# Optimization experiments

Hardware: AMD Instinct MI355X
Metric: run time of the kernel (lower is better)

Reference implementation:

```python
import jax, jax.numpy as jnp
import numpy as np
import math

HEADS = 16
D_MODEL = 1024
EPS = 1e-5  # nn.LayerNorm default


def setup_inputs() -> dict:
    key = jax.random.key(0)
    ks = jax.random.split(key, 12)
    bs, s, d = 4, 2048, D_MODEL
    scale = 1.0 / math.sqrt(d)
    inp = {
        "q": jax.random.normal(ks[0], (bs, s, d), jnp.float32),
        "k": jax.random.normal(ks[1], (bs, s, d), jnp.float32),
        "v": jax.random.normal(ks[2], (bs, s, d), jnp.float32),
        # causal target mask, broadcast over batch; 0 => masked
        "trg_mask": jnp.broadcast_to(jnp.tril(jnp.ones((s, s), jnp.int32)), (bs, s, s)),
        "Wq": jax.random.normal(ks[3], (d, d), jnp.float32) * scale,
        "bq": jax.random.normal(ks[4], (d,), jnp.float32) * 0.01,
        "Wk": jax.random.normal(ks[5], (d, d), jnp.float32) * scale,
        "bk": jax.random.normal(ks[6], (d,), jnp.float32) * 0.01,
        "Wv": jax.random.normal(ks[7], (d, d), jnp.float32) * scale,
        "bv": jax.random.normal(ks[8], (d,), jnp.float32) * 0.01,
        "gamma": jnp.ones((d,), jnp.float32),
        "beta": jnp.zeros((d,), jnp.float32),
    }
    return inp


def _layer_norm(x, gamma, beta):
    mu = jnp.mean(x, axis=-1, keepdims=True)
    var = jnp.mean(jnp.square(x - mu), axis=-1, keepdims=True)
    return (x - mu) * jax.lax.rsqrt(var + EPS) * gamma + beta


def reference(q, k, v, trg_mask, Wq, bq, Wk, bk, Wv, bv, gamma, beta):
    bs, s, d = q.shape
    h, dk = HEADS, d // HEADS
    temp = q
    # nn.Linear: x @ W.T + b
    qp = (q @ Wq.T + bq).reshape(bs, s, h, dk)
    kp = (k @ Wk.T + bk).reshape(bs, s, h, dk)
    vp = (v @ Wv.T + bv).reshape(bs, s, h, dk)
    # scores [bs, h, s, s]
    scores = jnp.einsum('bqhd,bkhd->bhqk', qp, kp)
    # NOTE: original masks BEFORE dividing by sqrt(dk)
    scores = jnp.where(trg_mask[:, None, :, :] == 0, jnp.float32(-1e9), scores)
    attn = jax.nn.softmax(scores / math.sqrt(dk), axis=-1)
    ctx = jnp.einsum('bhqk,bkhd->bqhd', attn, vp).reshape(bs, s, d)
    # (cat over heads == transpose-back merge, identical math)
    return _layer_norm(ctx + temp, gamma, beta)
```

## Files before the change

### kernel.cpp

```cpp
#include <hip/hip_runtime.h>
#include <hip/hip_bf16.h>
#include <stdint.h>

#define BATCH 4
#define SEQ 2048
#define DMODEL 1024
#define HEADS 16
#define DKH 64
#define MTOT (BATCH * SEQ)

typedef float  fx4  __attribute__((ext_vector_type(4)));
typedef short  sx8  __attribute__((ext_vector_type(8)));
typedef __bf16 bx8  __attribute__((ext_vector_type(8)));
typedef unsigned short ux4 __attribute__((ext_vector_type(4)));
typedef unsigned int   ux2i __attribute__((ext_vector_type(2)));
typedef unsigned int   ux4i __attribute__((ext_vector_type(4)));

__device__ __forceinline__ fx4 mfma16(sx8 a, sx8 b, fx4 c) {
  return __builtin_amdgcn_mfma_f32_16x16x32_bf16(
      __builtin_bit_cast(bx8, a), __builtin_bit_cast(bx8, b), c, 0, 0, 0);
}

__device__ __forceinline__ unsigned short f2bf(float x) {
  return __builtin_bit_cast(unsigned short, __float2bfloat16(x));
}

__device__ __forceinline__ float bf2f(unsigned short u) {
  return __builtin_bit_cast(float, (uint32_t)u << 16);
}

__device__ __forceinline__ void gll16(const void* g, void* l) {
  __builtin_amdgcn_global_load_lds(
      (const __attribute__((address_space(1))) void*)g,
      (__attribute__((address_space(3))) void*)l, 16, 0, 0);
}

__global__ __launch_bounds__(256) void convert_w(
    const float* __restrict__ s0, const float* __restrict__ s1, const float* __restrict__ s2,
    unsigned short* __restrict__ d0, unsigned short* __restrict__ d1, unsigned short* __restrict__ d2) {
  const float* s = (blockIdx.y == 0) ? s0 : (blockIdx.y == 1) ? s1 : s2;
  unsigned short* d = (blockIdx.y == 0) ? d0 : (blockIdx.y == 1) ? d1 : d2;
  const int n4 = DMODEL * DMODEL / 4;
  for (int i = blockIdx.x * 256 + threadIdx.x; i < n4; i += gridDim.x * 256) {
    fx4 v = ((const fx4*)s)[i];
    ux4 o;
    o.x = f2bf(v.x); o.y = f2bf(v.y); o.z = f2bf(v.z); o.w = f2bf(v.w);
    ((ux4*)d)[i] = o;
  }
}

#define GBM 128
#define GBN 128
#define GBK 64
#define NBLK ((MTOT / GBM) * (DMODEL / GBN))

struct QkvArgs {
  const float* A[3];
  const unsigned short* B[3];
  const float* bias[3];
  unsigned short* C[3];
  float cscale[3];
};

__global__ __launch_bounds__(256) void gemm_qkv(QkvArgs args) {
  const int e = blockIdx.z;
  const float* __restrict__ A = args.A[e];
  const unsigned short* __restrict__ B = args.B[e];
  const float* __restrict__ bias = args.bias[e];
  unsigned short* __restrict__ C = args.C[e];
  const float cscale = args.cscale[e];

  const int lin = blockIdx.x;
  const int swz = (lin & 7) * (NBLK / 8) + (lin >> 3);
  const int m0 = (swz >> 3) * GBM;
  const int n0 = (swz & 7) * GBN;

  __shared__ unsigned short As[GBM][GBK];
  __shared__ unsigned short Bs[GBN][GBK];

  const int tid  = threadIdx.x;
  const int lane = tid & 63;
  const int wv   = tid >> 6;
  const int wm   = wv >> 1;
  const int wn   = wv & 1;
  const int g    = lane >> 4;
  const int l16  = lane & 15;

  fx4 acc[4][4];
#pragma unroll
  for (int m = 0; m < 4; ++m)
#pragma unroll
    for (int n = 0; n < 4; ++n) acc[m][n] = (fx4){0.f, 0.f, 0.f, 0.f};

  for (int kt = 0; kt < DMODEL / GBK; ++kt) {
    const int k0 = kt * GBK;
#pragma unroll
    for (int i = 0; i < 4; ++i) {
      const int c = i * 256 + tid;
      const int row = c >> 3, col8 = c & 7;
      gll16(B + (size_t)(n0 + row) * DMODEL + k0 + col8 * 8, &Bs[0][0] + c * 8);
    }
#pragma unroll
    for (int i = 0; i < 4; ++i) {
      const int c = i * 256 + tid;
      const int row = c >> 3, col8 = c & 7;
      const float* src = A + (size_t)(m0 + row) * DMODEL + k0 + col8 * 8;
      fx4 a0 = *(const fx4*)src;
      fx4 a1 = *(const fx4*)(src + 4);
      sx8 pk;
      pk[0] = (short)f2bf(a0.x); pk[1] = (short)f2bf(a0.y);
      pk[2] = (short)f2bf(a0.z); pk[3] = (short)f2bf(a0.w);
      pk[4] = (short)f2bf(a1.x); pk[5] = (short)f2bf(a1.y);
      pk[6] = (short)f2bf(a1.z); pk[7] = (short)f2bf(a1.w);
      *(sx8*)(&As[0][0] + c * 8) = pk;
    }
    __syncthreads();

    sx8 af[4][2], bfr[4][2];
#pragma unroll
    for (int m = 0; m < 4; ++m)
#pragma unroll
      for (int kc = 0; kc < 2; ++kc)
        af[m][kc] = *(const sx8*)(&As[wm * 64 + m * 16 + l16][kc * 32 + g * 8]);
#pragma unroll
    for (int n = 0; n < 4; ++n)
#pragma unroll
      for (int kc = 0; kc < 2; ++kc)
        bfr[n][kc] = *(const sx8*)(&Bs[wn * 64 + n * 16 + l16][kc * 32 + g * 8]);
#pragma unroll
    for (int kc = 0; kc < 2; ++kc)
#pragma unroll
      for (int m = 0; m < 4; ++m)
#pragma unroll
        for (int n = 0; n < 4; ++n)
          acc[m][n] = mfma16(af[m][kc], bfr[n][kc], acc[m][n]);
    __syncthreads();
  }

#pragma unroll
  for (int n = 0; n < 4; ++n) {
    const int gcol = n0 + wn * 64 + n * 16 + l16;
    const float bv = bias[gcol];
#pragma unroll
    for (int m = 0; m < 4; ++m) {
      const int grow = m0 + wm * 64 + m * 16 + g * 4;
#pragma unroll
      for (int r = 0; r < 4; ++r)
        C[(size_t)(grow + r) * DMODEL + gcol] = f2bf((acc[m][n][r] + bv) * cscale);
    }
  }
}

#define QBLK 128
#define KVB 64
#define NQT (SEQ / QBLK)
#define DEFER_THR 8.0f

__global__ __launch_bounds__(256) void attn(const unsigned short* __restrict__ qp,
                                            const unsigned short* __restrict__ kp,
                                            const unsigned short* __restrict__ vp,
                                            unsigned short* __restrict__ ctx) {
  const int gid = blockIdx.x;
  const int hb  = gid & 63;
  const int h   = hb >> 2;
  const int b   = hb & 3;
  const int qt  = (NQT - 1) - (gid >> 6);

  __shared__ unsigned short Ks[2][KVB][DKH];
  __shared__ unsigned short Vs[2][KVB * DKH];
  __shared__ unsigned short Ps[4][32][KVB + 2];

  const int tid  = threadIdx.x;
  const int lane = tid & 63;
  const int wv   = tid >> 6;
  const int g    = lane >> 4;
  const int l16  = lane & 15;

  const size_t bh = ((size_t)b * SEQ) * DMODEL + (size_t)h * DKH;
  const int sbase = (lane & 48) + ((lane & 48) >> 2);

  const int q0  = qt * QBLK;
  const int ntl = 2 * (qt + 1);
  const int wq0 = q0 + wv * 32;

  sx8 qf[2][2];
#pragma unroll
  for (int m = 0; m < 2; ++m)
#pragma unroll
    for (int kc = 0; kc < 2; ++kc)
      qf[m][kc] = *(const sx8*)(qp + bh + (size_t)(wq0 + m * 16 + l16) * DMODEL + kc * 32 + g * 8);

  fx4 oacc[2][4];
  float mrow[2], lrow[2];
#pragma unroll
  for (int m = 0; m < 2; ++m) {
#pragma unroll
    for (int nt = 0; nt < 4; ++nt) oacc[m][nt] = (fx4){0.f, 0.f, 0.f, 0.f};
    mrow[m] = -1e30f; lrow[m] = 0.f;
  }

#pragma unroll
  for (int i = 0; i < 2; ++i) {
    const int c = i * 256 + tid;
    {
      const int row = c >> 3, col8 = c & 7;
      gll16(kp + bh + (size_t)row * DMODEL + (col8 ^ (row & 7)) * 8, &Ks[0][0][0] + c * 8);
    }
    {
      const int kv = ((c >> 5) << 2) | ((c >> 1) & 3);
      const int d0 = (((c >> 3) & 3) << 4) | ((c & 1) << 3);
      gll16(vp + bh + (size_t)kv * DMODEL + d0, &Vs[0][0] + c * 8);
    }
  }
  __syncthreads();

  int cur = 0;
  for (int t = 0; t < ntl; ++t) {
    const int kv0 = t * KVB;

    if (t + 1 < ntl) {
#pragma unroll
      for (int i = 0; i < 2; ++i) {
        const int c = i * 256 + tid;
        {
          const int row = c >> 3, col8 = c & 7;
          gll16(kp + bh + (size_t)(kv0 + KVB + row) * DMODEL + (col8 ^ (row & 7)) * 8,
                &Ks[cur ^ 1][0][0] + c * 8);
        }
        {
          const int kv = ((c >> 5) << 2) | ((c >> 1) & 3);
          const int d0 = (((c >> 3) & 3) << 4) | ((c & 1) << 3);
          gll16(vp + bh + (size_t)(kv0 + KVB + kv) * DMODEL + d0, &Vs[cur ^ 1][0] + c * 8);
        }
      }
    }

    sx8 kf[4][2];
#pragma unroll
    for (int nt = 0; nt < 4; ++nt) {
      const int row = l16 + 16 * nt;
#pragma unroll
      for (int kc = 0; kc < 2; ++kc)
        kf[nt][kc] = *(const sx8*)(&Ks[cur][row][((kc * 4 + g) ^ (row & 7)) * 8]);
    }
    fx4 st[2][4];
#pragma unroll
    for (int m = 0; m < 2; ++m)
#pragma unroll
      for (int nt = 0; nt < 4; ++nt) st[m][nt] = (fx4){0.f, 0.f, 0.f, 0.f};
    __builtin_amdgcn_s_setprio(1);
#pragma unroll
    for (int kc = 0; kc < 2; ++kc)
#pragma unroll
      for (int m = 0; m < 2; ++m)
#pragma unroll
        for (int nt = 0; nt < 4; ++nt)
          st[m][nt] = mfma16(kf[nt][kc], qf[m][kc], st[m][nt]);
    __builtin_amdgcn_s_setprio(0);

    bool mlive[2];
#pragma unroll
    for (int m = 0; m < 2; ++m) {
      mlive[m] = (kv0 <= wq0 + m * 16 + 15);
      if (!mlive[m]) continue;
      const int qrow = wq0 + m * 16 + l16;
      if (kv0 + KVB - 1 > wq0 + m * 16) {
#pragma unroll
        for (int nt = 0; nt < 4; ++nt)
#pragma unroll
          for (int r = 0; r < 4; ++r) {
            const int kvc = kv0 + nt * 16 + g * 4 + r;
            st[m][nt][r] = (kvc <= qrow) ? st[m][nt][r] : -1e30f;
          }
      }
      float mx = -1e30f;
#pragma unroll
      for (int nt = 0; nt < 4; ++nt)
#pragma unroll
        for (int r = 0; r < 4; ++r) mx = fmaxf(mx, st[m][nt][r]);
      mx = fmaxf(mx, __shfl_xor(mx, 16));
      mx = fmaxf(mx, __shfl_xor(mx, 32));

      if (!__all(mx <= mrow[m] + DEFER_THR)) {
        const float mnew = fmaxf(mrow[m], mx);
        const float corr = exp2f(mrow[m] - mnew);
        mrow[m] = mnew;
        lrow[m] *= corr;
        float c4[4];
#pragma unroll
        for (int r = 0; r < 4; ++r) c4[r] = __shfl(corr, sbase + r, 64);
#pragma unroll
        for (int nt = 0; nt < 4; ++nt)
#pragma unroll
          for (int r = 0; r < 4; ++r) oacc[m][nt][r] *= c4[r];
      }

      float rsum = 0.f;
#pragma unroll
      for (int nt = 0; nt < 4; ++nt)
#pragma unroll
        for (int r = 0; r < 4; ++r) {
          const float p = exp2f(st[m][nt][r] - mrow[m]);
          st[m][nt][r] = p;
          rsum += p;
        }
      rsum += __shfl_xor(rsum, 16);
      rsum += __shfl_xor(rsum, 32);
      lrow[m] += rsum;

      const int prow = m * 16 + l16;
      char* psrow = (char*)&Ps[wv][prow][0];
#pragma unroll
      for (int nt = 0; nt < 4; ++nt)
#pragma unroll
        for (int rr = 0; rr < 2; ++rr) {
          const uint32_t pk = (uint32_t)f2bf(st[m][nt][2 * rr]) |
                              ((uint32_t)f2bf(st[m][nt][2 * rr + 1]) << 16);
          *(uint32_t*)(psrow + ((nt * 2 + (g >> 1)) ^ (prow & 7)) * 16 + (g & 1) * 8 + rr * 4) = pk;
        }
    }

    const uint32_t vsb = (uint32_t)(uintptr_t)&Vs[cur][0];
#pragma unroll
    for (int kc = 0; kc < 2; ++kc) {
      sx8 vf[4];
#pragma unroll
      for (int nt = 0; nt < 4; ++nt) {
        const uint32_t a = vsb + (uint32_t)((kc * 8 + g * 2) * 512 + nt * 128 + l16 * 8);
        ux2i r0, r1;
        asm volatile("ds_read_b64_tr_b16 %0, %2\n\t"
                     "ds_read_b64_tr_b16 %1, %2 offset:512"
                     : "=&v"(r0), "=&v"(r1) : "v"(a));
        ux4i tmp;
        tmp[0] = r0[0]; tmp[1] = r0[1]; tmp[2] = r1[0]; tmp[3] = r1[1];
        vf[nt] = __builtin_bit_cast(sx8, tmp);
      }
      asm volatile("s_waitcnt lgkmcnt(0)" ::: "memory");
      __builtin_amdgcn_sched_barrier(0);
      __builtin_amdgcn_s_setprio(1);
#pragma unroll
      for (int m = 0; m < 2; ++m) {
        if (!mlive[m]) continue;
        const int prow = m * 16 + l16;
        sx8 pf = *(const sx8*)(&Ps[wv][prow][((kc * 4 + g) ^ (prow & 7)) * 8]);
#pragma unroll
        for (int nt = 0; nt < 4; ++nt)
          oacc[m][nt] = mfma16(pf, vf[nt], oacc[m][nt]);
      }
      __builtin_amdgcn_s_setprio(0);
    }

    __syncthreads();
    cur ^= 1;
  }

#pragma unroll
  for (int m = 0; m < 2; ++m) {
    const float inv = 1.0f / lrow[m];
    float i4[4];
#pragma unroll
    for (int r = 0; r < 4; ++r) i4[r] = __shfl(inv, sbase + r, 64);
#pragma unroll
    for (int nt = 0; nt < 4; ++nt)
#pragma unroll
      for (int r = 0; r < 4; ++r)
        ctx[bh + (size_t)(wq0 + m * 16 + g * 4 + r) * DMODEL + nt * 16 + l16] =
            f2bf(oacc[m][nt][r] * i4[r]);
  }
}

__global__ __launch_bounds__(256) void ln_kernel(const unsigned short* __restrict__ ctxb,
                                                 const float* __restrict__ qin,
                                                 float* __restrict__ out,
                                                 const float* __restrict__ gamma,
                                                 const float* __restrict__ beta) {
  const int row = blockIdx.x;
  const int tid = threadIdx.x;
  const unsigned short* crow = ctxb + (size_t)row * DMODEL;
  const float* qr = qin + (size_t)row * DMODEL;
  float* orow = out + (size_t)row * DMODEL;

  ux4 cv = ((const ux4*)crow)[tid];
  fx4 qv = ((const fx4*)qr)[tid];
  fx4 x;
  x.x = bf2f(cv.x) + qv.x;
  x.y = bf2f(cv.y) + qv.y;
  x.z = bf2f(cv.z) + qv.z;
  x.w = bf2f(cv.w) + qv.w;

  float s  = x.x + x.y + x.z + x.w;
  float ss = x.x * x.x + x.y * x.y + x.z * x.z + x.w * x.w;
#pragma unroll
  for (int off = 1; off < 64; off <<= 1) {
    s  += __shfl_xor(s, off);
    ss += __shfl_xor(ss, off);
  }
  __shared__ float rs[4], rss[4];
  if ((tid & 63) == 0) { rs[tid >> 6] = s; rss[tid >> 6] = ss; }
  __syncthreads();
  s  = rs[0] + rs[1] + rs[2] + rs[3];
  ss = rss[0] + rss[1] + rss[2] + rss[3];

  const float mu   = s * (1.0f / DMODEL);
  const float var  = ss * (1.0f / DMODEL) - mu * mu;
  const float rstd = rsqrtf(var + 1e-5f);

  fx4 gv = ((const fx4*)gamma)[tid];
  fx4 bv = ((const fx4*)beta)[tid];
  fx4 o;
  o.x = (x.x - mu) * rstd * gv.x + bv.x;
  o.y = (x.y - mu) * rstd * gv.y + bv.y;
  o.z = (x.z - mu) * rstd * gv.z + bv.z;
  o.w = (x.w - mu) * rstd * gv.w + bv.w;
  ((fx4*)orow)[tid] = o;
}

extern "C" void kernel_launch(void* const* d_in, const int* in_sizes, int n_in,
                              void* d_out, int out_size, void* d_ws, size_t ws_size,
                              hipStream_t stream) {
  const float* q     = (const float*)d_in[0];
  const float* k     = (const float*)d_in[1];
  const float* v     = (const float*)d_in[2];
  const float* Wq    = (const float*)d_in[4];
  const float* bq    = (const float*)d_in[5];
  const float* Wk    = (const float*)d_in[6];
  const float* bk    = (const float*)d_in[7];
  const float* Wv    = (const float*)d_in[8];
  const float* bv    = (const float*)d_in[9];
  const float* gamma = (const float*)d_in[10];
  const float* beta  = (const float*)d_in[11];

  unsigned short* Wqb  = (unsigned short*)d_ws;
  unsigned short* Wkb  = Wqb + (size_t)DMODEL * DMODEL;
  unsigned short* Wvb  = Wkb + (size_t)DMODEL * DMODEL;
  unsigned short* qpj  = Wvb + (size_t)DMODEL * DMODEL;
  unsigned short* kpj  = qpj + (size_t)MTOT * DMODEL;
  unsigned short* vpj  = kpj + (size_t)MTOT * DMODEL;
  unsigned short* ctxb = vpj + (size_t)MTOT * DMODEL;

  convert_w<<<dim3(256, 3), 256, 0, stream>>>(Wq, Wk, Wv, Wqb, Wkb, Wvb);

  QkvArgs ga;
  ga.A[0] = q;   ga.A[1] = k;   ga.A[2] = v;
  ga.B[0] = Wqb; ga.B[1] = Wkb; ga.B[2] = Wvb;
  ga.bias[0] = bq; ga.bias[1] = bk; ga.bias[2] = bv;
  ga.C[0] = qpj; ga.C[1] = kpj; ga.C[2] = vpj;
  ga.cscale[0] = 0.125f * 1.4426950408889634f;
  ga.cscale[1] = 1.0f;
  ga.cscale[2] = 1.0f;
  gemm_qkv<<<dim3(NBLK, 1, 3), 256, 0, stream>>>(ga);

  attn<<<dim3(NQT * HEADS * BATCH), 256, 0, stream>>>(qpj, kpj, vpj, ctxb);

  ln_kernel<<<MTOT, 256, 0, stream>>>(ctxb, q, (float*)d_out, gamma, beta);
}
```

Measured before the change: 203.7 us.

## Double attention query tile to 256 rows with 512-thread blocks

The attention query block grows from 128 to 256 rows and the block grows to 8 waves, so each K/V tile loaded into shared memory serves twice as many query rows. Each thread now issues a single K and V load per tile instead of two, and the grid shrinks to half as many blocks. This cuts K/V global traffic. In exchange there are fewer blocks to fill the GPU, a coarser causal tail (diagonal blocks do more masked work), and bigger blocks that may lower occupancy. Whether the unseen mask and diagonal handling stays correct with the new tile geometry is uncertain.

```diff
diff --git a/kernel.cpp b/kernel.cpp
--- a/kernel.cpp
+++ b/kernel.cpp
@@ -151,12 +151,12 @@
   }
 }
 
-#define QBLK 128
+#define QBLK 256
 #define KVB 64
 #define NQT (SEQ / QBLK)
 #define DEFER_THR 8.0f
 
-__global__ __launch_bounds__(256) void attn(const unsigned short* __restrict__ qp,
+__global__ __launch_bounds__(512) void attn(const unsigned short* __restrict__ qp,
                                             const unsigned short* __restrict__ kp,
                                             const unsigned short* __restrict__ vp,
                                             unsigned short* __restrict__ ctx) {
@@ -168,7 +168,7 @@
 
   __shared__ unsigned short Ks[2][KVB][DKH];
   __shared__ unsigned short Vs[2][KVB * DKH];
-  __shared__ unsigned short Ps[4][32][KVB + 2];
+  __shared__ unsigned short Ps[8][32][KVB + 2];
 
   const int tid  = threadIdx.x;
   const int lane = tid & 63;
@@ -180,7 +180,7 @@
   const int sbase = (lane & 48) + ((lane & 48) >> 2);
 
   const int q0  = qt * QBLK;
-  const int ntl = 2 * (qt + 1);
+  const int ntl = (q0 + QBLK) / KVB;
   const int wq0 = q0 + wv * 32;
 
   sx8 qf[2][2];
@@ -199,19 +199,12 @@
     mrow[m] = -1e30f; lrow[m] = 0.f;
   }
 
-#pragma unroll
-  for (int i = 0; i < 2; ++i) {
-    const int c = i * 256 + tid;
-    {
-      const int row = c >> 3, col8 = c & 7;
-      gll16(kp + bh + (size_t)row * DMODEL + (col8 ^ (row & 7)) * 8, &Ks[0][0][0] + c * 8);
-    }
-    {
-      const int kv = ((c >> 5) << 2) | ((c >> 1) & 3);
-      const int d0 = (((c >> 3) & 3) << 4) | ((c & 1) << 3);
-      gll16(vp + bh + (size_t)kv * DMODEL + d0, &Vs[0][0] + c * 8);
-    }
-  }
+  const int krow  = tid >> 3, kcol8 = tid & 7;
+  const int vkv   = ((tid >> 5) << 2) | ((tid >> 1) & 3);
+  const int vd0   = (((tid >> 3) & 3) << 4) | ((tid & 1) << 3);
+
+  gll16(kp + bh + (size_t)krow * DMODEL + (kcol8 ^ (krow & 7)) * 8, &Ks[0][0][0] + tid * 8);
+  gll16(vp + bh + (size_t)vkv * DMODEL + vd0, &Vs[0][0] + tid * 8);
   __syncthreads();
 
   int cur = 0;
@@ -219,20 +212,9 @@
     const int kv0 = t * KVB;
 
     if (t + 1 < ntl) {
-#pragma unroll
-      for (int i = 0; i < 2; ++i) {
-        const int c = i * 256 + tid;
-        {
-          const int row = c >> 3, col8 = c & 7;
-          gll16(kp + bh + (size_t)(kv0 + KVB + row) * DMODEL + (col8 ^ (row & 7)) * 8,
-                &Ks[cur ^ 1][0][0] + c * 8);
-        }
-        {
-          const int kv = ((c >> 5) << 2) | ((c >> 1) & 3);
-          const int d0 = (((c >> 3) & 3) << 4) | ((c & 1) << 3);
-          gll16(vp + bh + (size_t)(kv0 + KVB + kv) * DMODEL + d0, &Vs[cur ^ 1][0] + c * 8);
-        }
-      }
+      gll16(kp + bh + (size_t)(kv0 + KVB + krow) * DMODEL + (kcol8 ^ (krow & 7)) * 8,
+            &Ks[cur ^ 1][0][0] + tid * 8);
+      gll16(vp + bh + (size_t)(kv0 + KVB + vkv) * DMODEL + vd0, &Vs[cur ^ 1][0] + tid * 8);
     }
 
     sx8 kf[4][2];
@@ -450,7 +432,7 @@
   ga.cscale[2] = 1.0f;
   gemm_qkv<<<dim3(NBLK, 1, 3), 256, 0, stream>>>(ga);
 
-  attn<<<dim3(NQT * HEADS * BATCH), 256, 0, stream>>>(qpj, kpj, vpj, ctxb);
+  attn<<<dim3(NQT * HEADS * BATCH), 512, 0, stream>>>(qpj, kpj, vpj, ctxb);
 
   ln_kernel<<<MTOT, 256, 0, stream>>>(ctxb, q, (float*)d_out, gamma, beta);
 }
```

After: 212.8 us. +4.5%, slower.

## Double-buffer QKV GEMM shared tiles and prefetch next K-tile during MFMA

Applied to the files above, without the earlier changes.

The QKV projection GEMM now keeps two LDS buffers for A and B. It issues global loads for the next K-tile (direct-to-LDS for B, register staging for fp32 A) before running the current tile's MFMAs, then converts and stores A after the compute. One barrier per iteration replaces two, and s_setprio raises wave priority around the MFMA block. This is meant to hide global-load latency behind the matrix math, at the cost of doubled LDS (64KB) and extra registers for the prefetched A values, which may reduce occupancy.

```diff
diff --git a/kernel.cpp b/kernel.cpp
--- a/kernel.cpp
+++ b/kernel.cpp
@@ -53,6 +53,7 @@
 #define GBN 128
 #define GBK 64
 #define NBLK ((MTOT / GBM) * (DMODEL / GBN))
+#define NKT  (DMODEL / GBK)
 
 struct QkvArgs {
   const float* A[3];
@@ -75,8 +76,8 @@
   const int m0 = (swz >> 3) * GBM;
   const int n0 = (swz & 7) * GBN;
 
-  __shared__ unsigned short As[GBM][GBK];
-  __shared__ unsigned short Bs[GBN][GBK];
+  __shared__ unsigned short As[2][GBM][GBK];
+  __shared__ unsigned short Bs[2][GBN][GBK];
 
   const int tid  = threadIdx.x;
   const int lane = tid & 63;
@@ -86,47 +87,64 @@
   const int g    = lane >> 4;
   const int l16  = lane & 15;
 
+  const int srow  = tid >> 3;
+  const int scol8 = tid & 7;
+  const float* agp = A + (size_t)(m0 + srow) * DMODEL + scol8 * 8;
+  const unsigned short* bgp = B + (size_t)(n0 + srow) * DMODEL + scol8 * 8;
+
   fx4 acc[4][4];
 #pragma unroll
   for (int m = 0; m < 4; ++m)
 #pragma unroll
     for (int n = 0; n < 4; ++n) acc[m][n] = (fx4){0.f, 0.f, 0.f, 0.f};
 
-  for (int kt = 0; kt < DMODEL / GBK; ++kt) {
-    const int k0 = kt * GBK;
-#pragma unroll
-    for (int i = 0; i < 4; ++i) {
-      const int c = i * 256 + tid;
-      const int row = c >> 3, col8 = c & 7;
-      gll16(B + (size_t)(n0 + row) * DMODEL + k0 + col8 * 8, &Bs[0][0] + c * 8);
-    }
-#pragma unroll
-    for (int i = 0; i < 4; ++i) {
-      const int c = i * 256 + tid;
-      const int row = c >> 3, col8 = c & 7;
-      const float* src = A + (size_t)(m0 + row) * DMODEL + k0 + col8 * 8;
-      fx4 a0 = *(const fx4*)src;
-      fx4 a1 = *(const fx4*)(src + 4);
-      sx8 pk;
-      pk[0] = (short)f2bf(a0.x); pk[1] = (short)f2bf(a0.y);
-      pk[2] = (short)f2bf(a0.z); pk[3] = (short)f2bf(a0.w);
-      pk[4] = (short)f2bf(a1.x); pk[5] = (short)f2bf(a1.y);
-      pk[6] = (short)f2bf(a1.z); pk[7] = (short)f2bf(a1.w);
-      *(sx8*)(&As[0][0] + c * 8) = pk;
-    }
-    __syncthreads();
+#pragma unroll
+  for (int i = 0; i < 4; ++i)
+    gll16(bgp + (size_t)(i * 32) * DMODEL, &Bs[0][0][0] + (i * 256 + tid) * 8);
+#pragma unroll
+  for (int i = 0; i < 4; ++i) {
+    const float* src = agp + (size_t)(i * 32) * DMODEL;
+    fx4 a0 = *(const fx4*)src;
+    fx4 a1 = *(const fx4*)(src + 4);
+    sx8 pk;
+    pk[0] = (short)f2bf(a0.x); pk[1] = (short)f2bf(a0.y);
+    pk[2] = (short)f2bf(a0.z); pk[3] = (short)f2bf(a0.w);
+    pk[4] = (short)f2bf(a1.x); pk[5] = (short)f2bf(a1.y);
+    pk[6] = (short)f2bf(a1.z); pk[7] = (short)f2bf(a1.w);
+    *(sx8*)(&As[0][0][0] + (i * 256 + tid) * 8) = pk;
+  }
+  __syncthreads();
+
+  for (int kt = 0; kt < NKT; ++kt) {
+    const int cur = kt & 1;
+    const bool more = (kt + 1 < NKT);
+
+    fx4 a0n[4], a1n[4];
+    if (more) {
+      const int k1 = (kt + 1) * GBK;
+#pragma unroll
+      for (int i = 0; i < 4; ++i)
+        gll16(bgp + (size_t)(i * 32) * DMODEL + k1, &Bs[cur ^ 1][0][0] + (i * 256 + tid) * 8);
+#pragma unroll
+      for (int i = 0; i < 4; ++i) {
+        const float* src = agp + (size_t)(i * 32) * DMODEL + k1;
+        a0n[i] = *(const fx4*)src;
+        a1n[i] = *(const fx4*)(src + 4);
+      }
+    }
 
     sx8 af[4][2], bfr[4][2];
 #pragma unroll
     for (int m = 0; m < 4; ++m)
 #pragma unroll
       for (int kc = 0; kc < 2; ++kc)
-        af[m][kc] = *(const sx8*)(&As[wm * 64 + m * 16 + l16][kc * 32 + g * 8]);
+        af[m][kc] = *(const sx8*)(&As[cur][wm * 64 + m * 16 + l16][kc * 32 + g * 8]);
 #pragma unroll
     for (int n = 0; n < 4; ++n)
 #pragma unroll
       for (int kc = 0; kc < 2; ++kc)
-        bfr[n][kc] = *(const sx8*)(&Bs[wn * 64 + n * 16 + l16][kc * 32 + g * 8]);
+        bfr[n][kc] = *(const sx8*)(&Bs[cur][wn * 64 + n * 16 + l16][kc * 32 + g * 8]);
+    __builtin_amdgcn_s_setprio(1);
 #pragma unroll
     for (int kc = 0; kc < 2; ++kc)
 #pragma unroll
@@ -134,6 +152,19 @@
 #pragma unroll
         for (int n = 0; n < 4; ++n)
           acc[m][n] = mfma16(af[m][kc], bfr[n][kc], acc[m][n]);
+    __builtin_amdgcn_s_setprio(0);
+
+    if (more) {
+#pragma unroll
+      for (int i = 0; i < 4; ++i) {
+        sx8 pk;
+        pk[0] = (short)f2bf(a0n[i].x); pk[1] = (short)f2bf(a0n[i].y);
+        pk[2] = (short)f2bf(a0n[i].z); pk[3] = (short)f2bf(a0n[i].w);
+        pk[4] = (short)f2bf(a1n[i].x); pk[5] = (short)f2bf(a1n[i].y);
+        pk[6] = (short)f2bf(a1n[i].z); pk[7] = (short)f2bf(a1n[i].w);
+        *(sx8*)(&As[cur ^ 1][0][0] + (i * 256 + tid) * 8) = pk;
+      }
+    }
     __syncthreads();
   }
 
```

Result: slower. 210.8 us (+3.5%).
